# Kernel optimization log

Measured on AMD Instinct MI355X. Metric: run time of the kernel, lower is better.

## Reference

```python
import jax, jax.numpy as jnp
import numpy as np

IN_FEATURE = 4096
OUT_FEATURE = 4096
BLOCK_SIZE = 128
NUM_BLOCKS = IN_FEATURE // BLOCK_SIZE


def setup_inputs() -> dict:
    key = jax.random.key(0)
    k1, k2 = jax.random.split(key)
    x = jax.random.normal(k1, (4, 2048, IN_FEATURE), dtype=jnp.float32)
    # weight laid out as the original nn.Linear: [out_feature, in_feature]
    weight = jax.random.normal(k2, (OUT_FEATURE, IN_FEATURE), dtype=jnp.float32) * (1.0 / np.sqrt(IN_FEATURE))
    return {"x": x, "weight": weight}


def reference(x, weight):
    # The grouped 1x1 conv + reduce-sum over blocks is exactly a blockwise
    # matmul summed over blocks, i.e. out = x @ weight.T.
    # Expressed per-block to mirror the original structure without the
    # conv/permute/reshape overhead:
    b, s, in_f = x.shape
    xb = x.reshape(b, s, NUM_BLOCKS, BLOCK_SIZE)            # [b,s,nb,k]
    wb = weight.reshape(OUT_FEATURE, NUM_BLOCKS, BLOCK_SIZE)  # [o,nb,k]
    # sum over blocks (nb) and block_size (k) == full contraction over in_feature
    out = jnp.einsum('bsnk,onk->bso', xb, wb)
    return out
```

## Files before the change

kernel.cpp:

```cpp
#include <hip/hip_runtime.h>
#include <hip/hip_bf16.h>
#include <stdint.h>


typedef __bf16 bf16x8 __attribute__((ext_vector_type(8)));
typedef float f32x4 __attribute__((ext_vector_type(4)));

__device__ __forceinline__ unsigned short f2bf(float f) {
  unsigned u = __builtin_bit_cast(unsigned, f);
  u += 0x7FFFu + ((u >> 16) & 1u);
  return (unsigned short)(u >> 16);
}

__global__ void cvt_f32_to_bf16(const float* __restrict__ src,
                                unsigned short* __restrict__ dst, long n4) {
  long i = (long)blockIdx.x * blockDim.x + threadIdx.x;
  const long stride = (long)gridDim.x * blockDim.x;
  for (; i < n4; i += stride) {
    float4 v = reinterpret_cast<const float4*>(src)[i];
    ushort4 o;
    o.x = f2bf(v.x); o.y = f2bf(v.y); o.z = f2bf(v.z); o.w = f2bf(v.w);
    reinterpret_cast<ushort4*>(dst)[i] = o;
  }
}

__device__ __forceinline__ void gload_lds16(const void* g, void* lds) {
  __builtin_amdgcn_global_load_lds(
      (__attribute__((address_space(1))) void*)(g),
      (__attribute__((address_space(3))) void*)(lds), 16, 0, 0);
}

#define BARRIER()                                    \
  do {                                               \
    asm volatile("" ::: "memory");                   \
    __builtin_amdgcn_s_barrier();                    \
    asm volatile("" ::: "memory");                   \
  } while (0)
#define WAIT_VM4() asm volatile("s_waitcnt vmcnt(4)" ::: "memory")
#define WAIT_VM0() asm volatile("s_waitcnt vmcnt(0)" ::: "memory")

#define READ_A(AB, LO)                                                      \
  _Pragma("unroll") for (int mi = 0; mi < 4; ++mi) {                        \
    const int row_ = ((LO)*4 + mi) * 16 + lr;                               \
    fa[(LO)*4 + mi][0] = *(const bf16x8*)((AB) + row_ * 128 + sx0);         \
    fa[(LO)*4 + mi][1] = *(const bf16x8*)((AB) + row_ * 128 + sx1);         \
  }
#define READ_B(BB, LO)                                                      \
  _Pragma("unroll") for (int ni = 0; ni < 2; ++ni) {                        \
    const int row_ = brow0 + ((LO)*2 + ni) * 16 + lr;                       \
    fb[(LO)*2 + ni][0] = *(const bf16x8*)((BB) + row_ * 128 + sx0);         \
    fb[(LO)*2 + ni][1] = *(const bf16x8*)((BB) + row_ * 128 + sx1);         \
  }
#define MQ(M0, N0)                                                          \
  _Pragma("unroll") for (int kk = 0; kk < 2; ++kk)                          \
  _Pragma("unroll") for (int mi = 0; mi < 4; ++mi)                          \
  _Pragma("unroll") for (int ni = 0; ni < 2; ++ni)                          \
      acc[(M0) + mi][(N0) + ni] = __builtin_amdgcn_mfma_f32_16x16x32_bf16(  \
          fa[(M0) + mi][kk], fb[(N0) + ni][kk], acc[(M0) + mi][(N0) + ni],  \
          0, 0, 0);

#define PH(READS, STAGES, M0, N0, WAITS)  \
  do {                                    \
    READS STAGES                          \
    __builtin_amdgcn_s_setprio(1);        \
    MQ(M0, N0)                            \
    __builtin_amdgcn_s_setprio(0);        \
    WAITS BARRIER();                      \
  } while (0)

__global__ __launch_bounds__(512, 2) void gemm256(
    const unsigned short* __restrict__ A, const unsigned short* __restrict__ B,
    float* __restrict__ C, int M, int N, int K) {
  __shared__ __attribute__((aligned(1024))) char lds[131072];
  const int A00 = 0, A01 = 16384, A10 = 32768, A11 = 49152;
  const int B00 = 65536, B01 = 81920, B10 = 98304, B11 = 114688;

  const int t = threadIdx.x;
  const int l = t & 63;
  const int w = t >> 6;
  const int wm = w >> 2;
  const int wn = w & 3;
  const int q = l >> 4;
  const int lr = l & 15;
  const int xc = (lr & 7) << 4;
  const int sx0 = (q * 16) ^ xc;
  const int sx1 = (64 + q * 16) ^ xc;
  const int brow0 = (wn & 1) * 64;
  const int srow = l >> 3;
  const int sslot = ((l & 7) ^ ((l >> 3) & 7)) * 8;

  const int nwg = gridDim.x;
  int swz = blockIdx.x;
  if ((nwg & 7) == 0) swz = (swz & 7) * (nwg >> 3) + (swz >> 3);
  const int ntx = N >> 8;
  const int bx = swz % ntx;
  const int by = swz / ntx;
  const int mBase = by * 256, nBase = bx * 256;

  const char* Ard0 = lds + wm * 16384;
  const char* Ard1 = lds + 32768 + wm * 16384;
  const char* Brd0 = lds + 65536 + (wn >> 1) * 16384;
  const char* Brd1 = lds + 98304 + (wn >> 1) * 16384;

  bf16x8 fa[8][2], fb[4][2];
  f32x4 acc[8][4] = {};

  auto STAGE = [&](const unsigned short* __restrict__ G, int row0, int k0,
                   int ldsOff) {
    const unsigned short* s =
        G + (size_t)(row0 + w * 8 + srow) * K + k0 + sslot;
    char* d = lds + ldsOff + w * 1024;
    gload_lds16(s, d);
    gload_lds16(s + (size_t)64 * K, d + 8192);
  };

  STAGE(A, mBase, 0, A00);
  STAGE(A, mBase + 128, 0, A01);
  STAGE(B, nBase, 0, B00);
  STAGE(B, nBase + 128, 0, B01);
  STAGE(B, nBase, 64, B10);
  STAGE(A, mBase, 64, A10);
  WAIT_VM4();
  BARRIER();

  const int itermain = K / 128 - 1;
  for (int i = 0; i < itermain; ++i) {
    const int kA = (2 * i + 1) * 64;
    const int kB = kA + 64;
    const int kC = kB + 64;
    PH(READ_A(Ard0, 0) READ_B(Brd0, 0), STAGE(A, mBase + 128, kA, A11);, 0, 0, );
    PH(READ_B(Brd0, 1),                 STAGE(B, nBase + 128, kA, B11);, 0, 2, );
    PH(READ_A(Ard0, 1),                 STAGE(B, nBase,       kB, B00);, 4, 0, );
    PH(,                                STAGE(A, mBase,       kB, A00);, 4, 2, WAIT_VM4(););
    PH(READ_A(Ard1, 0) READ_B(Brd1, 0), STAGE(A, mBase + 128, kB, A01);, 0, 0, );
    PH(READ_B(Brd1, 1),                 STAGE(B, nBase + 128, kB, B01);, 0, 2, );
    PH(READ_A(Ard1, 1),                 STAGE(B, nBase,       kC, B10);, 4, 0, );
    PH(,                                STAGE(A, mBase,       kC, A10);, 4, 2, WAIT_VM4(););
  }

  {
    const int kT = K - 64;
    PH(READ_A(Ard0, 0) READ_B(Brd0, 0), STAGE(A, mBase + 128, kT, A11);, 0, 0, );
    PH(READ_B(Brd0, 1),                 STAGE(B, nBase + 128, kT, B11);, 0, 2, );
    PH(READ_A(Ard0, 1),                 ,                                4, 0, );
    PH(,                                ,                                4, 2, WAIT_VM0(););
    PH(READ_A(Ard1, 0) READ_B(Brd1, 0), ,                                0, 0, );
    PH(READ_B(Brd1, 1),                 ,                                0, 2, );
    PH(READ_A(Ard1, 1),                 ,                                4, 0, );
    PH(,                                ,                                4, 2, );
  }

  float* Cw = C + (size_t)(mBase + wm * 128 + q * 4) * N + nBase + wn * 64 + lr;
#pragma unroll
  for (int mi = 0; mi < 8; ++mi)
#pragma unroll
    for (int ni = 0; ni < 4; ++ni)
#pragma unroll
      for (int r = 0; r < 4; ++r)
        Cw[(size_t)(mi * 16 + r) * N + ni * 16] = acc[mi][ni][r];
}

typedef unsigned short ushort8f __attribute__((ext_vector_type(8)));
__global__ __launch_bounds__(256) void gemm_fb(
    const float* __restrict__ Af, const float* __restrict__ Wf,
    float* __restrict__ C, int M, int N, int K) {
  __shared__ __attribute__((aligned(16))) unsigned short Ash[128 * 64];
  __shared__ __attribute__((aligned(16))) unsigned short Bsh[128 * 64];
  const int t = threadIdx.x, l = t & 63, w = t >> 6;
  const int mBase = blockIdx.y * 128, nBase = blockIdx.x * 128;
  const int wm = w >> 1, wn = w & 1;
  const int lr = l & 15, lk = (l >> 4) * 8;
  f32x4 acc[4][4] = {};
  const int frow = t >> 1, fkh = (t & 1) * 32;
  for (int k0 = 0; k0 < K; k0 += 64) {
    const float* ga = Af + (size_t)(mBase + frow) * K + k0 + fkh;
    const float* gb = Wf + (size_t)(nBase + frow) * K + k0 + fkh;
#pragma unroll
    for (int j = 0; j < 4; ++j) {
      float4 a0 = reinterpret_cast<const float4*>(ga)[2 * j];
      float4 a1 = reinterpret_cast<const float4*>(ga)[2 * j + 1];
      float4 b0 = reinterpret_cast<const float4*>(gb)[2 * j];
      float4 b1 = reinterpret_cast<const float4*>(gb)[2 * j + 1];
      ushort8f oa = {f2bf(a0.x), f2bf(a0.y), f2bf(a0.z), f2bf(a0.w),
                     f2bf(a1.x), f2bf(a1.y), f2bf(a1.z), f2bf(a1.w)};
      ushort8f ob = {f2bf(b0.x), f2bf(b0.y), f2bf(b0.z), f2bf(b0.w),
                     f2bf(b1.x), f2bf(b1.y), f2bf(b1.z), f2bf(b1.w)};
      *reinterpret_cast<ushort8f*>(&Ash[frow * 64 + fkh + j * 8]) = oa;
      *reinterpret_cast<ushort8f*>(&Bsh[frow * 64 + fkh + j * 8]) = ob;
    }
    __syncthreads();
#pragma unroll
    for (int kk = 0; kk < 2; ++kk) {
      bf16x8 a[4], b[4];
#pragma unroll
      for (int mi = 0; mi < 4; ++mi)
        a[mi] = *reinterpret_cast<const bf16x8*>(
            &Ash[(wm * 64 + mi * 16 + lr) * 64 + kk * 32 + lk]);
#pragma unroll
      for (int ni = 0; ni < 4; ++ni)
        b[ni] = *reinterpret_cast<const bf16x8*>(
            &Bsh[(wn * 64 + ni * 16 + lr) * 64 + kk * 32 + lk]);
#pragma unroll
      for (int mi = 0; mi < 4; ++mi)
#pragma unroll
        for (int ni = 0; ni < 4; ++ni)
          acc[mi][ni] = __builtin_amdgcn_mfma_f32_16x16x32_bf16(
              a[mi], b[ni], acc[mi][ni], 0, 0, 0);
    }
    __syncthreads();
  }
  const int crow0 = mBase + wm * 64 + (l >> 4) * 4;
  const int ccol0 = nBase + wn * 64 + lr;
#pragma unroll
  for (int mi = 0; mi < 4; ++mi)
#pragma unroll
    for (int ni = 0; ni < 4; ++ni)
#pragma unroll
      for (int r = 0; r < 4; ++r)
        C[(size_t)(crow0 + mi * 16 + r) * N + ccol0 + ni * 16] =
            acc[mi][ni][r];
}

extern "C" void kernel_launch(void* const* d_in, const int* in_sizes, int n_in,
                              void* d_out, int out_size, void* d_ws, size_t ws_size,
                              hipStream_t stream) {
  (void)n_in; (void)out_size;
  const float* x = (const float*)d_in[0];
  const float* wgt = (const float*)d_in[1];
  float* out = (float*)d_out;

  const long x_elems = in_sizes[0];
  const long w_elems = in_sizes[1];
  const int K = 4096;
  const int M = (int)(x_elems / K);
  const int N = (int)(w_elems / K);

  const size_t need = (size_t)(x_elems + w_elems) * sizeof(unsigned short);
  const bool ok256 =
      (M % 256 == 0) && (N % 256 == 0) && (K % 128 == 0) && (K >= 256) &&
      ws_size >= need;
  if (ok256) {
    unsigned short* Abf = (unsigned short*)d_ws;
    unsigned short* Wbf = Abf + x_elems;
    cvt_f32_to_bf16<<<2048, 256, 0, stream>>>(x, Abf, x_elems / 4);
    cvt_f32_to_bf16<<<2048, 256, 0, stream>>>(wgt, Wbf, w_elems / 4);
    gemm256<<<dim3((M / 256) * (N / 256)), 512, 0, stream>>>(Abf, Wbf, out, M,
                                                             N, K);
  } else {
    dim3 grid(N / 128, M / 128);
    gemm_fb<<<grid, 256, 0, stream>>>(x, wgt, out, M, N, K);
  }
}
```

Measured before the change: 267.5 us.

## Merge eight pipeline phases into four with paired stages per barrier

Restructures the main-loop schedule of the 256x256 bf16 GEMM from eight phases per iteration to four. Each phase now issues two global-to-LDS stages and runs twice as many MFMAs, and the staging order changes so whole A or B k-slabs load together. This halves the workgroup barriers per iteration and is meant to cut sync overhead. The risk is longer phases with more register pressure and a changed LDS buffer reuse order, which could create hazards if the wait counts no longer match.

Measured after the change: 269.6 us. Within noise of the previous version (+0.8%).

```diff
diff --git a/kernel.cpp b/kernel.cpp
--- a/kernel.cpp
+++ b/kernel.cpp
@@ -59,11 +59,11 @@
           fa[(M0) + mi][kk], fb[(N0) + ni][kk], acc[(M0) + mi][(N0) + ni],  \
           0, 0, 0);
 
-#define PH(READS, STAGES, M0, N0, WAITS)  \
+#define PH(READS, STAGES, MQS, WAITS)     \
   do {                                    \
     READS STAGES                          \
     __builtin_amdgcn_s_setprio(1);        \
-    MQ(M0, N0)                            \
+    MQS                                   \
     __builtin_amdgcn_s_setprio(0);        \
     WAITS BARRIER();                      \
   } while (0)
@@ -119,7 +119,7 @@
   STAGE(B, nBase, 0, B00);
   STAGE(B, nBase + 128, 0, B01);
   STAGE(B, nBase, 64, B10);
-  STAGE(A, mBase, 64, A10);
+  STAGE(B, nBase + 128, 64, B11);
   WAIT_VM4();
   BARRIER();
 
@@ -128,26 +128,29 @@
     const int kA = (2 * i + 1) * 64;
     const int kB = kA + 64;
     const int kC = kB + 64;
-    PH(READ_A(Ard0, 0) READ_B(Brd0, 0), STAGE(A, mBase + 128, kA, A11);, 0, 0, );
-    PH(READ_B(Brd0, 1),                 STAGE(B, nBase + 128, kA, B11);, 0, 2, );
-    PH(READ_A(Ard0, 1),                 STAGE(B, nBase,       kB, B00);, 4, 0, );
-    PH(,                                STAGE(A, mBase,       kB, A00);, 4, 2, WAIT_VM4(););
-    PH(READ_A(Ard1, 0) READ_B(Brd1, 0), STAGE(A, mBase + 128, kB, A01);, 0, 0, );
-    PH(READ_B(Brd1, 1),                 STAGE(B, nBase + 128, kB, B01);, 0, 2, );
-    PH(READ_A(Ard1, 1),                 STAGE(B, nBase,       kC, B10);, 4, 0, );
-    PH(,                                STAGE(A, mBase,       kC, A10);, 4, 2, WAIT_VM4(););
+    PH(READ_A(Ard0, 0) READ_B(Brd0, 0) READ_B(Brd0, 1),
+       STAGE(A, mBase, kA, A10); STAGE(A, mBase + 128, kA, A11);,
+       MQ(0, 0) MQ(0, 2), );
+    PH(READ_A(Ard0, 1),
+       STAGE(B, nBase, kB, B00); STAGE(B, nBase + 128, kB, B01);,
+       MQ(4, 0) MQ(4, 2), WAIT_VM4(););
+    PH(READ_A(Ard1, 0) READ_B(Brd1, 0) READ_B(Brd1, 1),
+       STAGE(A, mBase, kB, A00); STAGE(A, mBase + 128, kB, A01);,
+       MQ(0, 0) MQ(0, 2), );
+    PH(READ_A(Ard1, 1),
+       STAGE(B, nBase, kC, B10); STAGE(B, nBase + 128, kC, B11);,
+       MQ(4, 0) MQ(4, 2), WAIT_VM4(););
   }
 
   {
     const int kT = K - 64;
-    PH(READ_A(Ard0, 0) READ_B(Brd0, 0), STAGE(A, mBase + 128, kT, A11);, 0, 0, );
-    PH(READ_B(Brd0, 1),                 STAGE(B, nBase + 128, kT, B11);, 0, 2, );
-    PH(READ_A(Ard0, 1),                 ,                                4, 0, );
-    PH(,                                ,                                4, 2, WAIT_VM0(););
-    PH(READ_A(Ard1, 0) READ_B(Brd1, 0), ,                                0, 0, );
-    PH(READ_B(Brd1, 1),                 ,                                0, 2, );
-    PH(READ_A(Ard1, 1),                 ,                                4, 0, );
-    PH(,                                ,                                4, 2, );
+    PH(READ_A(Ard0, 0) READ_B(Brd0, 0) READ_B(Brd0, 1),
+       STAGE(A, mBase, kT, A10); STAGE(A, mBase + 128, kT, A11);,
+       MQ(0, 0) MQ(0, 2), );
+    PH(READ_A(Ard0, 1), , MQ(4, 0) MQ(4, 2), WAIT_VM0(););
+    PH(READ_A(Ard1, 0) READ_B(Brd1, 0) READ_B(Brd1, 1), ,
+       MQ(0, 0) MQ(0, 2), );
+    PH(READ_A(Ard1, 1), , MQ(4, 0) MQ(4, 2), );
   }
 
   float* Cw = C + (size_t)(mBase + wm * 128 + q * 4) * N + nBase + wn * 64 + lr;
```
